# Optimization experiments

Hardware: AMD Instinct MI355X
Metric: run time of the kernel (lower is better)

The kernel has to match this reference:

```python
import jax, jax.numpy as jnp
import numpy as np

B, N, M = 4, 1024, 4096
DQ, DC = 1024, 1024
H, DH = 16, 64
INNER = H * DH
SCALE = DH ** -0.5


def setup_inputs() -> dict:
    key = jax.random.key(0)
    ks = jax.random.split(key, 6)
    x = jax.random.normal(ks[0], (B, N, DQ), dtype=jnp.float32)
    context = jax.random.normal(ks[1], (B, M, DC), dtype=jnp.float32)
    mask = jax.random.bernoulli(ks[2], 0.9, (B, M))  # bool, True = keep
    # weights, scaled like default torch Linear init (~1/sqrt(fan_in))
    Wq = jax.random.normal(ks[3], (DQ, INNER), dtype=jnp.float32) / np.sqrt(DQ)
    Wkv = jax.random.normal(ks[4], (DC, 2 * INNER), dtype=jnp.float32) / np.sqrt(DC)
    Wo = jax.random.normal(ks[5], (INNER, DQ), dtype=jnp.float32) / np.sqrt(INNER)
    bo = jnp.zeros((DQ,), dtype=jnp.float32)
    return {"x": x, "context": context, "mask": mask,
            "Wq": Wq, "Wkv": Wkv, "Wo": Wo, "bo": bo}


def reference(x, context, mask, Wq, Wkv, Wo, bo):
    # projections
    q = x @ Wq                     # [b, n, h*d]
    kv = context @ Wkv             # [b, m, 2*h*d]
    k, v = jnp.split(kv, 2, axis=-1)
    # split heads: [b, s, h*d] -> [b, h, s, d]
    def heads(t):
        b, s, _ = t.shape
        return t.reshape(b, s, H, DH).transpose(0, 2, 1, 3)
    q, k, v = heads(q), heads(k), heads(v)
    sim = jnp.einsum('bhid,bhjd->bhij', q, k) * SCALE   # [b, h, n, m]
    max_neg = -jnp.finfo(sim.dtype).max
    sim = jnp.where(mask[:, None, None, :], sim, max_neg)
    sim = jnp.clip(sim, -5.0, 5.0)  # masked entries become exactly -5
    attn = jax.nn.softmax(sim, axis=-1)
    out = jnp.einsum('bhij,bhjd->bhid', attn, v)        # [b, h, n, d]
    out = out.transpose(0, 2, 1, 3).reshape(x.shape[0], x.shape[1], INNER)
    return out @ Wo + bo
```

## Files before the change

### kernel.cpp

```cpp
#include <hip/hip_runtime.h>
#include <hip/hip_bf16.h>


typedef __attribute__((ext_vector_type(8))) short short8;
typedef __attribute__((ext_vector_type(8))) unsigned short u16x8;
typedef __attribute__((ext_vector_type(4))) float f32x4;
typedef __attribute__((ext_vector_type(16))) float f32x16;

static __device__ __forceinline__ void gload_lds16(const void* g, void* l) {
  __builtin_amdgcn_global_load_lds((const __attribute__((address_space(1))) void*)g,
                                   (__attribute__((address_space(3))) void*)l, 16, 0, 0);
}

static __device__ __forceinline__ unsigned short f2bf(float f) {
  __hip_bfloat16 h = __float2bfloat16(f);
  unsigned short u;
  __builtin_memcpy(&u, &h, 2);
  return u;
}

static __device__ __forceinline__ float bf2f(unsigned short u) {
  unsigned int x = (unsigned int)u << 16;
  float f;
  __builtin_memcpy(&f, &x, 4);
  return f;
}

static __device__ __forceinline__ unsigned int pack_rnd(float a, float b) {
  unsigned int ua, ub;
  __builtin_memcpy(&ua, &a, 4);
  __builtin_memcpy(&ub, &b, 4);
  return __builtin_amdgcn_perm(ua + 0x8000u, ub + 0x8000u, 0x03020706u);
}

__global__ __launch_bounds__(256) void cast_bf16_kernel(const float* __restrict__ in,
                                                        unsigned short* __restrict__ out,
                                                        int n8) {
  int idx = blockIdx.x * 256 + threadIdx.x;
  int stride = gridDim.x * 256;
  for (int i = idx; i < n8; i += stride) {
    const float4* p = (const float4*)in + (size_t)i * 2;
    float4 a = p[0], b = p[1];
    u16x8 r;
    r[0] = f2bf(a.x); r[1] = f2bf(a.y); r[2] = f2bf(a.z); r[3] = f2bf(a.w);
    r[4] = f2bf(b.x); r[5] = f2bf(b.y); r[6] = f2bf(b.z); r[7] = f2bf(b.w);
    *((u16x8*)out + i) = r;
  }
}

__global__ __launch_bounds__(256) void mask_bias_kernel(const int* __restrict__ mask,
                                                        float* __restrict__ bias, int n) {
  int i = blockIdx.x * 256 + threadIdx.x;
  if (i < n) bias[i] = mask[i] ? 0.0f : -1e30f;
}

__global__ __launch_bounds__(256) void transpose_cast_kernel(const float* __restrict__ W,
                                                             unsigned short* __restrict__ Wt,
                                                             int K, int N) {
  __shared__ float tile[32][33];
  int n0 = blockIdx.x * 32, k0 = blockIdx.y * 32;
  int tx = threadIdx.x & 31, ty = threadIdx.x >> 5;
#pragma unroll
  for (int r = 0; r < 32; r += 8)
    tile[ty + r][tx] = W[(size_t)(k0 + ty + r) * N + n0 + tx];
  __syncthreads();
#pragma unroll
  for (int r = 0; r < 32; r += 8)
    Wt[(size_t)(n0 + ty + r) * K + k0 + tx] = f2bf(tile[tx][ty + r]);
}

template <int EPI>
__global__ __launch_bounds__(256, 2) void gemm_bt_kernel(
    const unsigned short* __restrict__ A, const unsigned short* __restrict__ Bt,
    int M, int N, int K,
    unsigned short* __restrict__ out0, unsigned short* __restrict__ out1,
    float* __restrict__ outF, const float* __restrict__ bias) {
  __shared__ unsigned short As[128 * 64];
  __shared__ unsigned short Bs[128 * 64];
  const int tid = threadIdx.x;
  const int l = tid & 63;
  const int lq = l & 15, g = l >> 4;
  const int w = tid >> 6;
  const int wr = w >> 1, wc = w & 1;
  const int m0 = blockIdx.y * 128, n0 = blockIdx.x * 128;

  f32x4 acc[4][4] = {};

  for (int k0 = 0; k0 < K; k0 += 64) {
    __syncthreads();
#pragma unroll
    for (int t = 0; t < 4; ++t) {
      int c = t * 256 + tid;
      int row = c >> 3, cb = c & 7;
      int srcoff = (cb * 16) ^ ((row & 7) << 4);
      char* la = (char*)As + t * 4096 + (tid & 192) * 16;
      gload_lds16((const char*)(A + (size_t)(m0 + row) * K + k0) + srcoff, la);
      char* lb = (char*)Bs + t * 4096 + (tid & 192) * 16;
      gload_lds16((const char*)(Bt + (size_t)(n0 + row) * K + k0) + srcoff, lb);
    }
    __syncthreads();
#pragma unroll
    for (int ks = 0; ks < 2; ++ks) {
      short8 af[4], bfr[4];
#pragma unroll
      for (int mt = 0; mt < 4; ++mt) {
        int row = wr * 64 + mt * 16 + lq;
        af[mt] = *(const short8*)&As[row * 64 + ((ks * 32 + g * 8) ^ ((row & 7) << 3))];
      }
#pragma unroll
      for (int nt = 0; nt < 4; ++nt) {
        int row = wc * 64 + nt * 16 + lq;
        bfr[nt] = *(const short8*)&Bs[row * 64 + ((ks * 32 + g * 8) ^ ((row & 7) << 3))];
      }
#pragma unroll
      for (int mt = 0; mt < 4; ++mt)
#pragma unroll
        for (int nt = 0; nt < 4; ++nt)
          acc[mt][nt] =
              __builtin_amdgcn_mfma_f32_16x16x32_bf16(af[mt], bfr[nt], acc[mt][nt], 0, 0, 0);
    }
  }

#pragma unroll
  for (int mt = 0; mt < 4; ++mt) {
#pragma unroll
    for (int nt = 0; nt < 4; ++nt) {
      if (EPI == 1 && n0 >= 1024) {
        int colb = n0 - 1024 + wc * 64 + nt * 16 + lq;
        int h = colb >> 6, d = colb & 63;
        int rowb = m0 + wr * 64 + mt * 16 + g * 4;
        int b = rowb >> 12, mm = rowb & 4095;
        ushort4 pk;
        pk.x = f2bf(acc[mt][nt][0]);
        pk.y = f2bf(acc[mt][nt][1]);
        pk.z = f2bf(acc[mt][nt][2]);
        pk.w = f2bf(acc[mt][nt][3]);
        *(ushort4*)&out1[(((size_t)(b * 16 + h)) * 64 + d) * 4096 + mm] = pk;
      } else {
#pragma unroll
        for (int r = 0; r < 4; ++r) {
          int row = m0 + wr * 64 + mt * 16 + g * 4 + r;
          int col = n0 + wc * 64 + nt * 16 + lq;
          float v = acc[mt][nt][r];
          if (EPI == 0) {
            int b = row >> 10, nq = row & 1023;
            int h = col >> 6, d = col & 63;
            out0[(((size_t)(b * 16 + h)) * 1024 + nq) * 64 + d] =
                f2bf(v * 0.18033688011112042f);
          } else if (EPI == 1) {
            int b = row >> 12, mm = row & 4095;
            int h = col >> 6, d = col & 63;
            out0[(((size_t)(b * 16 + h)) * 4096 + mm) * 64 + d] = f2bf(v);
          } else {
            outF[(size_t)row * 1024 + col] = v + bias[col];
          }
        }
      }
    }
  }
}

__global__ __launch_bounds__(256, 3) void attn_kernel(
    const unsigned short* __restrict__ Q, const unsigned short* __restrict__ Kb,
    const unsigned short* __restrict__ VbT, const float* __restrict__ maskb,
    unsigned short* __restrict__ numP, float* __restrict__ denP) {
  __shared__ unsigned short Ks[64 * 64];
  __shared__ unsigned short Vt[64 * 64];

  const int tid = threadIdx.x;
  const int l = tid & 63, w = tid >> 6;
  const int lq = l & 31;
  const int hi = l >> 5;

  const int id = blockIdx.x;
  const int xcd = id & 7;
  const int kk = id >> 3;
  const int qi = kk & 7;
  const int pr = xcd * 32 + (kk >> 3);
  const int bh = pr & 63, js = pr >> 6;
  const int b = bh >> 4;
  const int q0 = qi * 128 + w * 32;

  const unsigned short* Qh = Q + (size_t)bh * 1024 * 64;
  const unsigned short* Kh = Kb + (size_t)bh * 4096 * 64;
  const unsigned short* Vth = VbT + (size_t)bh * 64 * 4096;
  const float* bb = maskb + b * 4096;

  const float CLIP2 = 7.213475204444817f;

  short8 qf[4];
#pragma unroll
  for (int kc = 0; kc < 4; ++kc)
    qf[kc] = *(const short8*)&Qh[(size_t)(q0 + lq) * 64 + kc * 16 + hi * 8];

  f32x16 oacc[2] = {};
  float den = 0.f;

  for (int jt = js * 16; jt < js * 16 + 16; ++jt) {
    const int j0 = jt * 64;
    __syncthreads();
#pragma unroll
    for (int t = 0; t < 2; ++t) {
      int c = t * 256 + tid;
      int row = c >> 3, cb = c & 7;
      int jrow = (row & 0x33) | ((row & 4) << 1) | ((row & 8) >> 1);
      int srcoff = (cb * 16) ^ ((row & 7) << 4);
      char* lk = (char*)Ks + t * 4096 + (tid & 192) * 16;
      gload_lds16((const char*)(Kh + (size_t)(j0 + jrow) * 64) + srcoff, lk);
    }
#pragma unroll
    for (int t = 0; t < 2; ++t) {
      int c = t * 256 + tid;
      int row = c >> 3, cb = c & 7;
      int srcoff = (cb * 16) ^ ((row & 7) << 4);
      char* lv = (char*)Vt + t * 4096 + (tid & 192) * 16;
      gload_lds16((const char*)(Vth + (size_t)row * 4096 + j0) + srcoff, lv);
    }
    __syncthreads();

#pragma unroll
    for (int half = 0; half < 2; ++half) {
      f32x16 sacc;
#pragma unroll
      for (int bq = 0; bq < 4; ++bq) {
        f32x4 m4 = *(const f32x4*)&bb[j0 + half * 32 + ((bq & 1) << 2) + (hi << 3) +
                                      ((bq >> 1) << 4)];
        sacc[bq * 4 + 0] = m4[0];
        sacc[bq * 4 + 1] = m4[1];
        sacc[bq * 4 + 2] = m4[2];
        sacc[bq * 4 + 3] = m4[3];
      }
#pragma unroll
      for (int kc = 0; kc < 4; ++kc) {
        int row = half * 32 + lq;
        short8 kf = *(const short8*)&Ks[row * 64 + ((kc * 16 + hi * 8) ^ ((row & 7) << 3))];
        sacc = __builtin_amdgcn_mfma_f32_32x32x16_bf16(kf, qf[kc], sacc, 0, 0, 0);
      }
#pragma unroll
      for (int r = 0; r < 16; ++r) {
        float v = fminf(fmaxf(sacc[r], -CLIP2), CLIP2);
        float p = exp2f(v);
        sacc[r] = p;
        den += p;
      }
      unsigned int wds[8];
#pragma unroll
      for (int i = 0; i < 8; ++i) wds[i] = pack_rnd(sacc[i * 2], sacc[i * 2 + 1]);
#pragma unroll
      for (int kt = 0; kt < 2; ++kt) {
        union { unsigned int u[4]; short8 s; } pa;
        pa.u[0] = wds[kt * 4 + 0];
        pa.u[1] = wds[kt * 4 + 1];
        pa.u[2] = wds[kt * 4 + 2];
        pa.u[3] = wds[kt * 4 + 3];
#pragma unroll
        for (int dt = 0; dt < 2; ++dt) {
          int row = dt * 32 + lq;
          short8 vf = *(const short8*)&Vt[row * 64 +
              ((half * 32 + kt * 16 + hi * 8) ^ ((row & 7) << 3))];
          oacc[dt] = __builtin_amdgcn_mfma_f32_32x32x16_bf16(pa.s, vf, oacc[dt], 0, 0, 0);
        }
      }
    }
  }

  den += __shfl_xor(den, 32);
  if (l < 32) denP[(((size_t)js * 64 + bh) * 1024) + q0 + l] = den;

#pragma unroll
  for (int dt = 0; dt < 2; ++dt)
#pragma unroll
    for (int r = 0; r < 16; ++r) {
      int q = q0 + (r & 3) + 8 * (r >> 2) + 4 * hi;
      int d = dt * 32 + lq;
      numP[((((size_t)js * 64 + bh) * 1024 + q) * 64) + d] = f2bf(oacc[dt][r]);
    }
}

__global__ __launch_bounds__(256) void attn_reduce_kernel(
    const unsigned short* __restrict__ numP, const float* __restrict__ denP,
    unsigned short* __restrict__ Ob) {
  int id = blockIdx.x * 256 + threadIdx.x;
  int d8 = id & 7;
  int q = (id >> 3) & 1023;
  int bh = id >> 13;
  int b = bh >> 4, h = bh & 15;
  float den = 0.f;
  float o[8] = {0.f, 0.f, 0.f, 0.f, 0.f, 0.f, 0.f, 0.f};
#pragma unroll
  for (int s = 0; s < 4; ++s) {
    const unsigned short* np =
        numP + ((((size_t)s * 64 + bh) * 1024 + q) * 64 + d8 * 8);
    u16x8 v = *(const u16x8*)np;
    den += denP[((size_t)s * 64 + bh) * 1024 + q];
#pragma unroll
    for (int e = 0; e < 8; ++e) o[e] += bf2f(v[e]);
  }
  float r = 1.0f / den;
  u16x8 outv;
#pragma unroll
  for (int e = 0; e < 8; ++e) outv[e] = f2bf(o[e] * r);
  *(u16x8*)&Ob[(((size_t)b * 1024 + q) * 1024) + h * 64 + d8 * 8] = outv;
}

extern "C" void kernel_launch(void* const* d_in, const int* in_sizes, int n_in,
                              void* d_out, int out_size, void* d_ws, size_t ws_size,
                              hipStream_t stream) {
  (void)in_sizes; (void)n_in; (void)out_size; (void)ws_size;
  const float* x    = (const float*)d_in[0];
  const float* ctx  = (const float*)d_in[1];
  const int*   mask = (const int*)d_in[2];
  const float* Wq   = (const float*)d_in[3];
  const float* Wkv  = (const float*)d_in[4];
  const float* Wo   = (const float*)d_in[5];
  const float* bo   = (const float*)d_in[6];
  float* out = (float*)d_out;

  char* ws = (char*)d_ws;
  const size_t MB = 1 << 20;
  unsigned short* numP = (unsigned short*)(ws + 0);
  float*          denP = (float*)(ws + 32 * MB);
  float*          mbias= (float*)(ws + 33 * MB);
  unsigned short* xb   = (unsigned short*)(ws + 0);
  unsigned short* cb   = (unsigned short*)(ws + 8 * MB);
  unsigned short* WqT  = (unsigned short*)(ws + 40 * MB);
  unsigned short* WkvT = (unsigned short*)(ws + 42 * MB);
  unsigned short* WoT  = (unsigned short*)(ws + 46 * MB);
  unsigned short* Qb   = (unsigned short*)(ws + 48 * MB);
  unsigned short* Kb   = (unsigned short*)(ws + 56 * MB);
  unsigned short* VbT  = (unsigned short*)(ws + 88 * MB);
  unsigned short* Ob   = (unsigned short*)(ws + 120 * MB);

  cast_bf16_kernel<<<2048, 256, 0, stream>>>(x, xb, (4 * 1024 * 1024) / 8);
  cast_bf16_kernel<<<2048, 256, 0, stream>>>(ctx, cb, (16 * 1024 * 1024) / 8);
  transpose_cast_kernel<<<dim3(32, 32), 256, 0, stream>>>(Wq, WqT, 1024, 1024);
  transpose_cast_kernel<<<dim3(64, 32), 256, 0, stream>>>(Wkv, WkvT, 1024, 2048);
  transpose_cast_kernel<<<dim3(32, 32), 256, 0, stream>>>(Wo, WoT, 1024, 1024);

  gemm_bt_kernel<0><<<dim3(8, 32), 256, 0, stream>>>(xb, WqT, 4096, 1024, 1024,
                                                     Qb, (unsigned short*)nullptr,
                                                     (float*)nullptr, (const float*)nullptr);
  gemm_bt_kernel<1><<<dim3(16, 128), 256, 0, stream>>>(cb, WkvT, 16384, 2048, 1024,
                                                       Kb, VbT,
                                                       (float*)nullptr, (const float*)nullptr);
  mask_bias_kernel<<<64, 256, 0, stream>>>(mask, mbias, 4 * 4096);
  attn_kernel<<<2048, 256, 0, stream>>>(Qb, Kb, VbT, mbias, numP, denP);
  attn_reduce_kernel<<<2048, 256, 0, stream>>>(numP, denP, Ob);
  gemm_bt_kernel<2><<<dim3(8, 32), 256, 0, stream>>>(Ob, WoT, 4096, 1024, 1024,
                                                     (unsigned short*)nullptr, (unsigned short*)nullptr,
                                                     out, bo);
}
```

Measured before the change: 271.5 us.

## Store K/V in d-blocked layout for conflict-free LDS reads; XCD-aware GEMM tile order

The KV projection epilogue now writes K as [bh][d/8][m][8] and V as [bh][m/8][d][8] blocks, so the attention kernel can load contiguous 1 KB slabs into LDS and read MFMA fragments with plain linear offsets instead of XOR-swizzled addressing. The GEMM kernel remaps block IDs so consecutive tiles land on the same XCD, aiming for better L2 reuse. The clamp now uses fmed3. The scattered 8-element epilogue writes may cost more in the GEMM, and the unswizzled LDS reads rely on the new layout to avoid bank conflicts.

Result: faster. 260.8 us (-3.9%).

```diff
diff --git a/kernel.cpp b/kernel.cpp
--- a/kernel.cpp
+++ b/kernel.cpp
@@ -82,7 +82,10 @@
   const int lq = l & 15, g = l >> 4;
   const int w = tid >> 6;
   const int wr = w >> 1, wc = w & 1;
-  const int m0 = blockIdx.y * 128, n0 = blockIdx.x * 128;
+  const int nwg = gridDim.x * gridDim.y;
+  const int idl = blockIdx.y * gridDim.x + blockIdx.x;
+  const int lin = (idl & 7) * (nwg >> 3) + (idl >> 3);
+  const int m0 = (lin / gridDim.x) * 128, n0 = (lin % gridDim.x) * 128;
 
   f32x4 acc[4][4] = {};
 
@@ -135,7 +138,8 @@
         pk.y = f2bf(acc[mt][nt][1]);
         pk.z = f2bf(acc[mt][nt][2]);
         pk.w = f2bf(acc[mt][nt][3]);
-        *(ushort4*)&out1[(((size_t)(b * 16 + h)) * 64 + d) * 4096 + mm] = pk;
+        size_t off = (((size_t)(b * 16 + h) * 512 + (mm >> 3)) * 64 + d) * 8 + (mm & 7);
+        *(ushort4*)&out1[off] = pk;
       } else {
 #pragma unroll
         for (int r = 0; r < 4; ++r) {
@@ -150,7 +154,8 @@
           } else if (EPI == 1) {
             int b = row >> 12, mm = row & 4095;
             int h = col >> 6, d = col & 63;
-            out0[(((size_t)(b * 16 + h)) * 4096 + mm) * 64 + d] = f2bf(v);
+            size_t off = (((size_t)(b * 16 + h) * 8 + (d >> 3)) * 4096 + mm) * 8 + (d & 7);
+            out0[off] = f2bf(v);
           } else {
             outF[(size_t)row * 1024 + col] = v + bias[col];
           }
@@ -161,11 +166,11 @@
 }
 
 __global__ __launch_bounds__(256, 3) void attn_kernel(
-    const unsigned short* __restrict__ Q, const unsigned short* __restrict__ Kb,
-    const unsigned short* __restrict__ VbT, const float* __restrict__ maskb,
+    const unsigned short* __restrict__ K2, const unsigned short* __restrict__ V2,
+    const unsigned short* __restrict__ Q, const float* __restrict__ maskb,
     unsigned short* __restrict__ numP, float* __restrict__ denP) {
-  __shared__ unsigned short Ks[64 * 64];
-  __shared__ unsigned short Vt[64 * 64];
+  __shared__ unsigned short Ks[8 * 64 * 8];
+  __shared__ unsigned short Vt[8 * 64 * 8];
 
   const int tid = threadIdx.x;
   const int l = tid & 63, w = tid >> 6;
@@ -182,8 +187,8 @@
   const int q0 = qi * 128 + w * 32;
 
   const unsigned short* Qh = Q + (size_t)bh * 1024 * 64;
-  const unsigned short* Kh = Kb + (size_t)bh * 4096 * 64;
-  const unsigned short* Vth = VbT + (size_t)bh * 64 * 4096;
+  const unsigned short* Kh = K2 + (size_t)bh * 8 * 4096 * 8;
+  const unsigned short* Vh = V2 + (size_t)bh * 512 * 64 * 8;
   const float* bb = maskb + b * 4096;
 
   const float CLIP2 = 7.213475204444817f;
@@ -202,19 +207,17 @@
 #pragma unroll
     for (int t = 0; t < 2; ++t) {
       int c = t * 256 + tid;
-      int row = c >> 3, cb = c & 7;
-      int jrow = (row & 0x33) | ((row & 4) << 1) | ((row & 8) >> 1);
-      int srcoff = (cb * 16) ^ ((row & 7) << 4);
+      int db = c >> 6, jj = c & 63;
+      int sig = (jj & 0x33) | ((jj & 4) << 1) | ((jj & 8) >> 1);
       char* lk = (char*)Ks + t * 4096 + (tid & 192) * 16;
-      gload_lds16((const char*)(Kh + (size_t)(j0 + jrow) * 64) + srcoff, lk);
+      gload_lds16((const char*)(Kh + ((size_t)db * 4096 + j0 + sig) * 8), lk);
     }
 #pragma unroll
     for (int t = 0; t < 2; ++t) {
       int c = t * 256 + tid;
-      int row = c >> 3, cb = c & 7;
-      int srcoff = (cb * 16) ^ ((row & 7) << 4);
+      int jb = c >> 6, d = c & 63;
       char* lv = (char*)Vt + t * 4096 + (tid & 192) * 16;
-      gload_lds16((const char*)(Vth + (size_t)row * 4096 + j0) + srcoff, lv);
+      gload_lds16((const char*)(Vh + ((size_t)((j0 >> 3) + jb) * 64 + d) * 8), lv);
     }
     __syncthreads();
 
@@ -232,13 +235,13 @@
       }
 #pragma unroll
       for (int kc = 0; kc < 4; ++kc) {
-        int row = half * 32 + lq;
-        short8 kf = *(const short8*)&Ks[row * 64 + ((kc * 16 + hi * 8) ^ ((row & 7) << 3))];
+        short8 kf = *(const short8*)((const char*)Ks + (2 * kc + hi) * 1024 +
+                                     (half * 32 + lq) * 16);
         sacc = __builtin_amdgcn_mfma_f32_32x32x16_bf16(kf, qf[kc], sacc, 0, 0, 0);
       }
 #pragma unroll
       for (int r = 0; r < 16; ++r) {
-        float v = fminf(fmaxf(sacc[r], -CLIP2), CLIP2);
+        float v = __builtin_amdgcn_fmed3f(sacc[r], -CLIP2, CLIP2);
         float p = exp2f(v);
         sacc[r] = p;
         den += p;
@@ -255,9 +258,8 @@
         pa.u[3] = wds[kt * 4 + 3];
 #pragma unroll
         for (int dt = 0; dt < 2; ++dt) {
-          int row = dt * 32 + lq;
-          short8 vf = *(const short8*)&Vt[row * 64 +
-              ((half * 32 + kt * 16 + hi * 8) ^ ((row & 7) << 3))];
+          short8 vf = *(const short8*)((const char*)Vt +
+              (4 * half + 2 * kt + hi) * 1024 + (dt * 32 + lq) * 16);
           oacc[dt] = __builtin_amdgcn_mfma_f32_32x32x16_bf16(pa.s, vf, oacc[dt], 0, 0, 0);
         }
       }
@@ -327,8 +329,8 @@
   unsigned short* WkvT = (unsigned short*)(ws + 42 * MB);
   unsigned short* WoT  = (unsigned short*)(ws + 46 * MB);
   unsigned short* Qb   = (unsigned short*)(ws + 48 * MB);
-  unsigned short* Kb   = (unsigned short*)(ws + 56 * MB);
-  unsigned short* VbT  = (unsigned short*)(ws + 88 * MB);
+  unsigned short* K2   = (unsigned short*)(ws + 56 * MB);
+  unsigned short* V2   = (unsigned short*)(ws + 88 * MB);
   unsigned short* Ob   = (unsigned short*)(ws + 120 * MB);
 
   cast_bf16_kernel<<<2048, 256, 0, stream>>>(x, xb, (4 * 1024 * 1024) / 8);
@@ -341,10 +343,10 @@
                                                      Qb, (unsigned short*)nullptr,
                                                      (float*)nullptr, (const float*)nullptr);
   gemm_bt_kernel<1><<<dim3(16, 128), 256, 0, stream>>>(cb, WkvT, 16384, 2048, 1024,
-                                                       Kb, VbT,
+                                                       K2, V2,
                                                        (float*)nullptr, (const float*)nullptr);
   mask_bias_kernel<<<64, 256, 0, stream>>>(mask, mbias, 4 * 4096);
-  attn_kernel<<<2048, 256, 0, stream>>>(Qb, Kb, VbT, mbias, numP, denP);
+  attn_kernel<<<2048, 256, 0, stream>>>(K2, V2, Qb, mbias, numP, denP);
   attn_reduce_kernel<<<2048, 256, 0, stream>>>(numP, denP, Ob);
   gemm_bt_kernel<2><<<dim3(8, 32), 256, 0, stream>>>(Ob, WoT, 4096, 1024, 1024,
                                                      (unsigned short*)nullptr, (unsigned short*)nullptr,
```
